# Optimization experiments

Hardware: AMD Instinct MI355X
Metric: run time of the kernel (lower is better)

Reference implementation:

```python
import jax, jax.numpy as jnp
import numpy as np
from jax import lax

NPOINT, RADIUS, NSAMPLE, K_KEY = 64, 1.0, 32, 64

def conv1d(x, W, b):
    # 1x1 Conv1d: x [B,Cin,N], W [Cout,Cin], b [Cout] -> [B,Cout,N]
    return jnp.einsum('bcn,dc->bdn', x, W) + b[None, :, None]

def farthest_point_sample(xyz, npoint):
    # xyz [B,N,3] -> idx [B,npoint]
    B, N, _ = xyz.shape
    dist0 = jnp.full((B, N), 1e10, dtype=xyz.dtype)
    far0 = jnp.zeros((B,), dtype=jnp.int32)
    def body(carry, _):
        dist, far = carry
        centroid = jnp.take_along_axis(xyz, far[:, None, None].astype(jnp.int32), axis=1)  # [B,1,3]
        d = jnp.sum((xyz - centroid) ** 2, -1)
        dist = jnp.minimum(dist, d)
        nxt = jnp.argmax(dist, -1).astype(jnp.int32)
        return (dist, nxt), far
    _, idxs = lax.scan(body, (dist0, far0), None, length=npoint)
    return idxs.T  # [B,npoint]

def ball_query(radius, nsample, xyz, new_xyz):
    # xyz [B,N,3], new_xyz [B,S,3] -> group_idx [B,S,nsample]
    N = xyz.shape[1]
    sqr = jnp.sum((new_xyz[:, :, None, :] - xyz[:, None, :, :]) ** 2, -1)  # [B,S,N]
    gidx = jnp.where(sqr > radius ** 2, N, jnp.arange(N, dtype=jnp.int32)[None, None, :])
    gidx = jnp.sort(gidx, axis=-1)[..., :nsample]
    first = gidx[..., :1]
    gidx = jnp.where(gidx == N, first, gidx)
    return gidx

def sample_and_group(npoint, radius, nsample, xyz, points):
    # xyz [B,N,3], points [B,N,D]
    B = xyz.shape[0]
    fps_idx = farthest_point_sample(xyz, npoint)                     # [B,S]
    bidx = jnp.arange(B)[:, None]
    new_xyz = xyz[bidx, fps_idx]                                     # [B,S,3]
    gidx = ball_query(radius, nsample, xyz, new_xyz)                 # [B,S,ns]
    bidx2 = jnp.arange(B)[:, None, None]
    grouped_xyz = xyz[bidx2, gidx]                                   # [B,S,ns,3]
    grouped_xyz_norm = grouped_xyz - new_xyz[:, :, None, :]
    grouped_points = points[bidx2, gidx]                             # [B,S,ns,D]
    new_points = jnp.concatenate([grouped_xyz_norm, grouped_points], axis=-1)
    return new_xyz, new_points

def setup_inputs() -> dict:
    key = jax.random.key(0)
    ks = jax.random.split(key, 12)
    B, C, N = 8, 6, 65536
    def w(k, co, ci):
        return jax.random.normal(k, (co, ci), jnp.float32) * (1.0 / np.sqrt(ci))
    return {
        'src_pts': jax.random.normal(ks[0], (B, C, N), jnp.float32),
        'tgt_pts': jax.random.normal(ks[1], (B, C, N), jnp.float32),
        'W1': w(ks[2], 32, 6),  'b1': jnp.zeros((32,), jnp.float32),
        'W2': w(ks[3], 64, 32), 'b2': jnp.zeros((64,), jnp.float32),
        'Wa': w(ks[4], 16, 64), 'ba': jnp.zeros((16,), jnp.float32),
        'Wb': w(ks[5], 8, 16),  'bb': jnp.zeros((8,), jnp.float32),
        'Wc': w(ks[6], 1, 8),   'bc': jnp.zeros((1,), jnp.float32),
    }

def reference(src_pts, tgt_pts, W1, b1, W2, b2, Wa, ba, Wb, bb, Wc, bc):
    # feat_extraction_layer: 1x1 conv stack over points -> deep per-point features
    h = jax.nn.relu(conv1d(src_pts, W1, b1))            # [B,32,N]
    deep_feat_pts = jax.nn.relu(conv1d(h, W2, b2))      # [B,64,N]
    # weighting_layer: per-point saliency weight + top-k keypoint indices (1-D, batch-0 idiom)
    w = jax.nn.relu(conv1d(deep_feat_pts, Wa, ba))
    w = jax.nn.relu(conv1d(w, Wb, bb))
    w = jax.nn.softplus(conv1d(w, Wc, bc))              # [B,1,N]
    _, keypts_idx = lax.top_k(w[0, 0], K_KEY)           # [K]
    # irregular keypoint gather (shared index across batch, as in src_pts[:, :, idx])
    src_keypts = src_pts[:, :, keypts_idx].transpose(0, 2, 1)   # [B,K,C]
    # ball-query sample_and_group on keypoints (computed then discarded, as in original)
    _gxyz, _gpts = sample_and_group(NPOINT, RADIUS, NSAMPLE, src_keypts[:, :, :3], src_keypts[:, :, 3:])
    return src_keypts
```

## Files before the change

### kernel.cpp

```cpp
#include <hip/hip_runtime.h>
#include <stdint.h>

#define N_PTS 65536
#define NB1 32768
#define NB2 4096
#define CAND_CAP 4096
#define FCAP 1024
typedef unsigned long long u64;


__global__ __launch_bounds__(256) void zero_kernel(uint4* __restrict__ z, int n4)
{
    const int i = blockIdx.x * 256 + threadIdx.x;
    const uint4 zz = {0u, 0u, 0u, 0u};
    if (i < n4) z[i] = zz;
}

__global__ __launch_bounds__(256, 2) void score_kernel(
    const float* __restrict__ src,
    const float* __restrict__ W1, const float* __restrict__ b1,
    const float* __restrict__ W2, const float* __restrict__ b2,
    const float* __restrict__ Wa, const float* __restrict__ ba,
    const float* __restrict__ Wb, const float* __restrict__ bb,
    const float* __restrict__ Wc, const float* __restrict__ bc,
    float* __restrict__ scores, unsigned* __restrict__ hist1)
{
    __shared__ unsigned histL[NB1 / 2];
    __shared__ __align__(16) float sW1[32 * 8];
    __shared__ __align__(16) float sW2[64 * 32];
    __shared__ __align__(16) float sWaT[64 * 16];
    __shared__ __align__(16) float sWb[8 * 16];
    __shared__ float sb2[64], sba[16], sbb[8], sWc[8], sbc1[1];
    const int t = threadIdx.x;

    {
        uint4* h4 = (uint4*)histL;
        const uint4 zz = {0u, 0u, 0u, 0u};
        #pragma unroll
        for (int i = 0; i < 16; i++) h4[t + 256 * i] = zz;
    }
    {
        const int j = t >> 3, c = t & 7;
        sW1[t] = (c < 6) ? W1[j * 6 + c] : ((c == 6) ? b1[j] : 0.f);
    }
    for (int i = t; i < 2048; i += 256) sW2[i] = W2[i];
    for (int i = t; i < 1024; i += 256) {
        const int j = i >> 4, q = i & 15;
        sWaT[i] = Wa[q * 64 + j];
    }
    if (t < 128) sWb[t] = Wb[t];
    if (t < 64)  sb2[t] = b2[t];
    if (t < 16)  sba[t] = ba[t];
    if (t < 8)   { sbb[t] = bb[t]; sWc[t] = Wc[t]; }
    if (t == 0)  sbc1[0] = bc[0];
    __syncthreads();

    const int p = blockIdx.x * 256 + t;

    float x[6];
    #pragma unroll
    for (int c = 0; c < 6; c++) x[c] = src[c * N_PTS + p];

    float h1[32];
    #pragma unroll
    for (int j = 0; j < 32; j++) {
        const float4 wA = *(const float4*)&sW1[j * 8];
        const float4 wB = *(const float4*)&sW1[j * 8 + 4];
        float a = wB.z;
        a = fmaf(wA.x, x[0], a); a = fmaf(wA.y, x[1], a);
        a = fmaf(wA.z, x[2], a); a = fmaf(wA.w, x[3], a);
        a = fmaf(wB.x, x[4], a); a = fmaf(wB.y, x[5], a);
        h1[j] = fmaxf(a, 0.f);
    }

    float h3[16];
    #pragma unroll
    for (int q = 0; q < 16; q++) h3[q] = sba[q];

    #pragma unroll 1
    for (int jb = 0; jb < 32; jb++) {
        const int j0 = 2 * jb, j1 = j0 + 1;
        const float4* r0 = (const float4*)&sW2[j0 * 32];
        const float4* r1 = (const float4*)&sW2[j1 * 32];
        const float4* wa0 = (const float4*)&sWaT[j0 * 16];
        const float4* wa1 = (const float4*)&sWaT[j1 * 16];
        float4 u[8], v[8], q0[4], q1[4];
        #pragma unroll
        for (int i = 0; i < 8; i++) u[i] = r0[i];
        #pragma unroll
        for (int i = 0; i < 8; i++) v[i] = r1[i];
        #pragma unroll
        for (int i = 0; i < 4; i++) q0[i] = wa0[i];
        #pragma unroll
        for (int i = 0; i < 4; i++) q1[i] = wa1[i];
        const float bj0 = sb2[j0], bj1 = sb2[j1];

        float a0 = 0.f, a1 = 0.f, a2 = 0.f, a3 = 0.f;
        float c0 = 0.f, c1 = 0.f, c2 = 0.f, c3 = 0.f;
        #pragma unroll
        for (int i4 = 0; i4 < 8; i4++) {
            const float h0 = h1[4 * i4 + 0], hh1 = h1[4 * i4 + 1];
            const float h2 = h1[4 * i4 + 2], hh3 = h1[4 * i4 + 3];
            a0 = fmaf(u[i4].x, h0, a0); a1 = fmaf(u[i4].y, hh1, a1);
            a2 = fmaf(u[i4].z, h2, a2); a3 = fmaf(u[i4].w, hh3, a3);
            c0 = fmaf(v[i4].x, h0, c0); c1 = fmaf(v[i4].y, hh1, c1);
            c2 = fmaf(v[i4].z, h2, c2); c3 = fmaf(v[i4].w, hh3, c3);
        }
        const float v0 = fmaxf((a0 + a1) + (a2 + a3) + bj0, 0.f);
        const float v1 = fmaxf((c0 + c1) + (c2 + c3) + bj1, 0.f);
        #pragma unroll
        for (int q4 = 0; q4 < 4; q4++) {
            float t0 = h3[4 * q4 + 0], t1 = h3[4 * q4 + 1];
            float t2 = h3[4 * q4 + 2], t3 = h3[4 * q4 + 3];
            t0 = fmaf(q0[q4].x, v0, t0); t1 = fmaf(q0[q4].y, v0, t1);
            t2 = fmaf(q0[q4].z, v0, t2); t3 = fmaf(q0[q4].w, v0, t3);
            t0 = fmaf(q1[q4].x, v1, t0); t1 = fmaf(q1[q4].y, v1, t1);
            t2 = fmaf(q1[q4].z, v1, t2); t3 = fmaf(q1[q4].w, v1, t3);
            h3[4 * q4 + 0] = t0; h3[4 * q4 + 1] = t1;
            h3[4 * q4 + 2] = t2; h3[4 * q4 + 3] = t3;
        }
    }
    #pragma unroll
    for (int q = 0; q < 16; q++) h3[q] = fmaxf(h3[q], 0.f);

    float z = sbc1[0];
    #pragma unroll
    for (int j = 0; j < 8; j++) {
        const float4* wbr = (const float4*)&sWb[j * 16];
        const float4 w0 = wbr[0], w1 = wbr[1], w2 = wbr[2], w3 = wbr[3];
        const float bj = sbb[j], wc = sWc[j];
        float s0 = bj, s1 = 0.f, s2 = 0.f, s3 = 0.f;
        s0 = fmaf(w0.x, h3[0],  s0); s1 = fmaf(w0.y, h3[1],  s1);
        s2 = fmaf(w0.z, h3[2],  s2); s3 = fmaf(w0.w, h3[3],  s3);
        s0 = fmaf(w1.x, h3[4],  s0); s1 = fmaf(w1.y, h3[5],  s1);
        s2 = fmaf(w1.z, h3[6],  s2); s3 = fmaf(w1.w, h3[7],  s3);
        s0 = fmaf(w2.x, h3[8],  s0); s1 = fmaf(w2.y, h3[9],  s1);
        s2 = fmaf(w2.z, h3[10], s2); s3 = fmaf(w2.w, h3[11], s3);
        s0 = fmaf(w3.x, h3[12], s0); s1 = fmaf(w3.y, h3[13], s1);
        s2 = fmaf(w3.z, h3[14], s2); s3 = fmaf(w3.w, h3[15], s3);
        z = fmaf(wc, fmaxf((s0 + s1) + (s2 + s3), 0.f), z);
    }

    {
        const float sp = fmaxf(z, 0.f) + log1pf(expf(-fabsf(z)));
        scores[p] = sp;
        const unsigned bin = __float_as_uint(sp) >> 16;
        atomicAdd(&histL[bin >> 1], 1u << (16 * (bin & 1)));
    }
    __syncthreads();

    {
        const uint4* h4 = (const uint4*)histL;
        for (int i = t; i < NB1 / 8; i += 256) {
            const uint4 v = h4[i];
            const int b0 = 8 * i;
            const unsigned w[4] = { v.x, v.y, v.z, v.w };
            #pragma unroll
            for (int k = 0; k < 4; k++) {
                const unsigned lo = w[k] & 0xFFFFu;
                const unsigned hi = w[k] >> 16;
                if (lo) atomicAdd(&hist1[b0 + 2 * k + 0], lo);
                if (hi) atomicAdd(&hist1[b0 + 2 * k + 1], hi);
            }
        }
    }
}

__global__ __launch_bounds__(256) void refine_kernel(
    const unsigned* __restrict__ hist1, const float* __restrict__ scores,
    unsigned* __restrict__ hist2, int* __restrict__ meta,
    u64* __restrict__ cand)
{
    __shared__ unsigned csum[256];
    __shared__ unsigned bsum[128];
    __shared__ int sh_c, sh_B;
    __shared__ unsigned sh_tail;
    const int t = threadIdx.x;

    {
        unsigned s = 0;
        const uint4* h4 = (const uint4*)(hist1 + t * 128);
        #pragma unroll
        for (int i = 0; i < 32; i++) {
            const uint4 v = h4[i];
            s += v.x + v.y + v.z + v.w;
        }
        csum[t] = s;
    }
    __syncthreads();
    for (int d = 1; d < 256; d <<= 1) {
        const unsigned v = (t + d < 256) ? csum[t + d] : 0u;
        __syncthreads();
        csum[t] += v;
        __syncthreads();
    }
    {
        const unsigned here = csum[t];
        const unsigned nxt = (t + 1 < 256) ? csum[t + 1] : 0u;
        if (here >= 64u && nxt < 64u) sh_c = t;
    }
    __syncthreads();
    const int cstar = sh_c;
    if (t < 128) bsum[t] = hist1[cstar * 128 + t];
    __syncthreads();
    {
        const unsigned ctail = (cstar + 1 < 256) ? csum[cstar + 1] : 0u;
        for (int d = 1; d < 128; d <<= 1) {
            unsigned v = 0u;
            if (t < 128 && t + d < 128) v = bsum[t + d];
            __syncthreads();
            if (t < 128) bsum[t] += v;
            __syncthreads();
        }
        if (t < 128) {
            const unsigned here = bsum[t] + ctail;
            const unsigned nxt = (t + 1 < 128) ? bsum[t + 1] + ctail : ctail;
            if (here >= 64u && nxt < 64u) { sh_B = cstar * 128 + t; sh_tail = nxt; }
        }
    }
    __syncthreads();
    const unsigned Bstar = (unsigned)sh_B;
    if (blockIdx.x == 0 && t == 0) { meta[0] = sh_B; meta[1] = (int)sh_tail; }

    const float4* s4 = (const float4*)scores;
    const int i = blockIdx.x * 256 + t;
    const float4 v = s4[i];
    const int n0 = 4 * i;
    #pragma unroll
    for (int k = 0; k < 4; k++) {
        const float sv = (k == 0) ? v.x : (k == 1) ? v.y : (k == 2) ? v.z : v.w;
        const unsigned b = __float_as_uint(sv);
        const unsigned hi = b >> 16;
        if (hi >= Bstar) {
            const int p = atomicAdd(&meta[2], 1);
            if (p < CAND_CAP) cand[p] = ((u64)b << 32) | (unsigned)~(n0 + k);
            if (hi == Bstar) atomicAdd(&hist2[(b & 0xFFFFu) >> 4], 1u);
        }
    }
}

__global__ __launch_bounds__(256) void final_kernel(
    const unsigned* __restrict__ hist2, const int* __restrict__ meta,
    const u64* __restrict__ cand, const float* __restrict__ src,
    float* __restrict__ out)
{
    __shared__ unsigned h2[NB2];
    __shared__ unsigned csum[256];
    __shared__ u64 keys[FCAP];
    __shared__ int idxs[64];
    __shared__ int sh_c, sh_T2, sh_cnt;
    const int t = threadIdx.x;
    const unsigned Bstar = (unsigned)meta[0];
    const unsigned tail1 = (unsigned)meta[1];

    {
        uint4* d = (uint4*)h2;
        const uint4* s = (const uint4*)hist2;
        #pragma unroll
        for (int i = 0; i < 4; i++) d[t + 256 * i] = s[t + 256 * i];
    }
    __syncthreads();

    {
        unsigned s = 0;
        #pragma unroll
        for (int i = 0; i < 16; i++) s += h2[t * 16 + i];
        csum[t] = s;
    }
    __syncthreads();
    for (int d = 1; d < 256; d <<= 1) {
        const unsigned v = (t + d < 256) ? csum[t + d] : 0u;
        __syncthreads();
        csum[t] += v;
        __syncthreads();
    }
    {
        const unsigned here = tail1 + csum[t];
        const unsigned nxt = tail1 + ((t + 1 < 256) ? csum[t + 1] : 0u);
        if (here >= 64u && nxt < 64u) sh_c = t;
    }
    __syncthreads();
    {
        const int c2 = sh_c;
        if (t == 0) {
            unsigned acc = tail1 + ((c2 + 1 < 256) ? csum[c2 + 1] : 0u);
            int T2 = c2 * 16;
            for (int b = c2 * 16 + 15; b >= c2 * 16; b--) {
                acc += h2[b];
                if (acc >= 64u) { T2 = b; break; }
            }
            sh_T2 = T2;
            sh_cnt = 0;
        }
    }
    __syncthreads();
    const unsigned T2 = (unsigned)sh_T2;

    int count = meta[2];
    if (count > CAND_CAP) count = CAND_CAP;
    for (int i = t; i < count; i += 256) {
        const u64 key = cand[i];
        const unsigned b = (unsigned)(key >> 32);
        const unsigned hi = b >> 16;
        if (hi > Bstar || ((b & 0xFFFFu) >> 4) >= T2) {
            const int p = atomicAdd(&sh_cnt, 1);
            if (p < FCAP) keys[p] = key;
        }
    }
    __syncthreads();

    int fcnt = sh_cnt;
    if (fcnt > FCAP) fcnt = FCAP;
    for (int i = t; i < fcnt; i += 256) {
        const u64 me = keys[i];
        int r = 0;
        for (int j = 0; j < fcnt; j++) r += (keys[j] > me);
        if (r < 64) idxs[r] = (int)~(unsigned)(me & 0xFFFFFFFFu);
    }
    __syncthreads();

    for (int e = t; e < 3072; e += 256) {
        const int b  = e / 384;
        const int rr = e % 384;
        const int kk = rr / 6;
        const int c  = rr % 6;
        out[e] = src[(b * 6 + c) * N_PTS + idxs[kk]];
    }
}

extern "C" void kernel_launch(void* const* d_in, const int* in_sizes, int n_in,
                              void* d_out, int out_size, void* d_ws, size_t ws_size,
                              hipStream_t stream)
{
    const float* src = (const float*)d_in[0];
    const float* W1 = (const float*)d_in[2];
    const float* b1 = (const float*)d_in[3];
    const float* W2 = (const float*)d_in[4];
    const float* b2 = (const float*)d_in[5];
    const float* Wa = (const float*)d_in[6];
    const float* ba = (const float*)d_in[7];
    const float* Wb = (const float*)d_in[8];
    const float* bb = (const float*)d_in[9];
    const float* Wc = (const float*)d_in[10];
    const float* bc = (const float*)d_in[11];

    char* ws = (char*)d_ws;
    float*    scores = (float*)ws;
    unsigned* hist1  = (unsigned*)(ws + 256 * 1024);
    unsigned* hist2  = (unsigned*)(ws + 384 * 1024);
    int*      meta   = (int*)(ws + 400 * 1024);
    u64*      cand   = (u64*)(ws + 408 * 1024);
    float*    out    = (float*)d_out;

    const int n4 = (NB1 + NB2 + 16) / 4;
    zero_kernel<<<(n4 + 255) / 256, 256, 0, stream>>>((uint4*)hist1, n4);
    score_kernel<<<256, 256, 0, stream>>>(src, W1, b1, W2, b2, Wa, ba,
                                          Wb, bb, Wc, bc, scores, hist1);
    refine_kernel<<<64, 256, 0, stream>>>(hist1, scores, hist2, meta, cand);
    final_kernel<<<1, 256, 0, stream>>>(hist2, meta, cand, src, out);
}
```

Baseline: 157.1 us.

## Pre-pack MLP weights in zero kernel and read them directly from global memory

The zero kernel gets an extra block that packs W1/b1, W2, transposed Wa and b2 into one interleaved buffer in the workspace. The score kernel drops its per-block LDS staging of weights and reads the uniform packed weights straight from global memory, where they should become scalar or cached loads. This removes LDS fill work and LDS weight reads per block, but depends on global loads of uniform data being served quickly from cache.

```diff
diff --git a/kernel.cpp b/kernel.cpp
--- a/kernel.cpp
+++ b/kernel.cpp
@@ -6,31 +6,52 @@
 #define NB2 4096
 #define CAND_CAP 4096
 #define FCAP 1024
+#define PK_FLOATS (256 + 32 * 112)
 typedef unsigned long long u64;
 
 
-__global__ __launch_bounds__(256) void zero_kernel(uint4* __restrict__ z, int n4)
-{
-    const int i = blockIdx.x * 256 + threadIdx.x;
+__global__ __launch_bounds__(256) void zero_pack_kernel(
+    uint4* __restrict__ z, int n4,
+    const float* __restrict__ W1, const float* __restrict__ b1,
+    const float* __restrict__ W2, const float* __restrict__ b2,
+    const float* __restrict__ Wa, float* __restrict__ pk)
+{
+    const int t = threadIdx.x;
+    const int i = blockIdx.x * 256 + t;
     const uint4 zz = {0u, 0u, 0u, 0u};
     if (i < n4) z[i] = zz;
+
+    if (blockIdx.x == gridDim.x - 1) {
+        for (int e = t; e < PK_FLOATS; e += 256) {
+            float v;
+            if (e < 256) {
+                const int j = e >> 3, c = e & 7;
+                v = (c < 6) ? W1[j * 6 + c] : ((c == 6) ? b1[j] : 0.f);
+            } else {
+                const int r = e - 256;
+                const int jb = r / 112, k = r % 112;
+                if (k < 32)       v = W2[(2 * jb) * 32 + k];
+                else if (k < 64)  v = W2[(2 * jb + 1) * 32 + (k - 32)];
+                else if (k < 80)  v = Wa[(k - 64) * 64 + 2 * jb];
+                else if (k < 96)  v = Wa[(k - 80) * 64 + (2 * jb + 1)];
+                else if (k == 96) v = b2[2 * jb];
+                else if (k == 97) v = b2[2 * jb + 1];
+                else              v = 0.f;
+            }
+            pk[e] = v;
+        }
+    }
 }
 
 __global__ __launch_bounds__(256, 2) void score_kernel(
     const float* __restrict__ src,
-    const float* __restrict__ W1, const float* __restrict__ b1,
-    const float* __restrict__ W2, const float* __restrict__ b2,
-    const float* __restrict__ Wa, const float* __restrict__ ba,
+    const float* __restrict__ pk,
+    const float* __restrict__ ba,
     const float* __restrict__ Wb, const float* __restrict__ bb,
     const float* __restrict__ Wc, const float* __restrict__ bc,
     float* __restrict__ scores, unsigned* __restrict__ hist1)
 {
     __shared__ unsigned histL[NB1 / 2];
-    __shared__ __align__(16) float sW1[32 * 8];
-    __shared__ __align__(16) float sW2[64 * 32];
-    __shared__ __align__(16) float sWaT[64 * 16];
-    __shared__ __align__(16) float sWb[8 * 16];
-    __shared__ float sb2[64], sba[16], sbb[8], sWc[8], sbc1[1];
     const int t = threadIdx.x;
 
     {
@@ -39,20 +60,6 @@
         #pragma unroll
         for (int i = 0; i < 16; i++) h4[t + 256 * i] = zz;
     }
-    {
-        const int j = t >> 3, c = t & 7;
-        sW1[t] = (c < 6) ? W1[j * 6 + c] : ((c == 6) ? b1[j] : 0.f);
-    }
-    for (int i = t; i < 2048; i += 256) sW2[i] = W2[i];
-    for (int i = t; i < 1024; i += 256) {
-        const int j = i >> 4, q = i & 15;
-        sWaT[i] = Wa[q * 64 + j];
-    }
-    if (t < 128) sWb[t] = Wb[t];
-    if (t < 64)  sb2[t] = b2[t];
-    if (t < 16)  sba[t] = ba[t];
-    if (t < 8)   { sbb[t] = bb[t]; sWc[t] = Wc[t]; }
-    if (t == 0)  sbc1[0] = bc[0];
     __syncthreads();
 
     const int p = blockIdx.x * 256 + t;
@@ -61,11 +68,12 @@
     #pragma unroll
     for (int c = 0; c < 6; c++) x[c] = src[c * N_PTS + p];
 
+    const float4* w1p = (const float4*)pk;
     float h1[32];
     #pragma unroll
     for (int j = 0; j < 32; j++) {
-        const float4 wA = *(const float4*)&sW1[j * 8];
-        const float4 wB = *(const float4*)&sW1[j * 8 + 4];
+        const float4 wA = w1p[2 * j];
+        const float4 wB = w1p[2 * j + 1];
         float a = wB.z;
         a = fmaf(wA.x, x[0], a); a = fmaf(wA.y, x[1], a);
         a = fmaf(wA.z, x[2], a); a = fmaf(wA.w, x[3], a);
@@ -73,27 +81,29 @@
         h1[j] = fmaxf(a, 0.f);
     }
 
+    const float4* bap = (const float4*)ba;
     float h3[16];
     #pragma unroll
-    for (int q = 0; q < 16; q++) h3[q] = sba[q];
+    for (int q4 = 0; q4 < 4; q4++) {
+        const float4 b4 = bap[q4];
+        h3[4 * q4 + 0] = b4.x; h3[4 * q4 + 1] = b4.y;
+        h3[4 * q4 + 2] = b4.z; h3[4 * q4 + 3] = b4.w;
+    }
 
     #pragma unroll 1
     for (int jb = 0; jb < 32; jb++) {
-        const int j0 = 2 * jb, j1 = j0 + 1;
-        const float4* r0 = (const float4*)&sW2[j0 * 32];
-        const float4* r1 = (const float4*)&sW2[j1 * 32];
-        const float4* wa0 = (const float4*)&sWaT[j0 * 16];
-        const float4* wa1 = (const float4*)&sWaT[j1 * 16];
+        const float4* blk = (const float4*)(pk + 256 + jb * 112);
         float4 u[8], v[8], q0[4], q1[4];
         #pragma unroll
-        for (int i = 0; i < 8; i++) u[i] = r0[i];
-        #pragma unroll
-        for (int i = 0; i < 8; i++) v[i] = r1[i];
-        #pragma unroll
-        for (int i = 0; i < 4; i++) q0[i] = wa0[i];
-        #pragma unroll
-        for (int i = 0; i < 4; i++) q1[i] = wa1[i];
-        const float bj0 = sb2[j0], bj1 = sb2[j1];
+        for (int i = 0; i < 8; i++) u[i] = blk[i];
+        #pragma unroll
+        for (int i = 0; i < 8; i++) v[i] = blk[8 + i];
+        #pragma unroll
+        for (int i = 0; i < 4; i++) q0[i] = blk[16 + i];
+        #pragma unroll
+        for (int i = 0; i < 4; i++) q1[i] = blk[20 + i];
+        const float bj0 = pk[256 + jb * 112 + 96];
+        const float bj1 = pk[256 + jb * 112 + 97];
 
         float a0 = 0.f, a1 = 0.f, a2 = 0.f, a3 = 0.f;
         float c0 = 0.f, c1 = 0.f, c2 = 0.f, c3 = 0.f;
@@ -123,12 +133,12 @@
     #pragma unroll
     for (int q = 0; q < 16; q++) h3[q] = fmaxf(h3[q], 0.f);
 
-    float z = sbc1[0];
+    float z = bc[0];
     #pragma unroll
     for (int j = 0; j < 8; j++) {
-        const float4* wbr = (const float4*)&sWb[j * 16];
+        const float4* wbr = (const float4*)(Wb + j * 16);
         const float4 w0 = wbr[0], w1 = wbr[1], w2 = wbr[2], w3 = wbr[3];
-        const float bj = sbb[j], wc = sWc[j];
+        const float bj = bb[j], wc = Wc[j];
         float s0 = bj, s1 = 0.f, s2 = 0.f, s3 = 0.f;
         s0 = fmaf(w0.x, h3[0],  s0); s1 = fmaf(w0.y, h3[1],  s1);
         s2 = fmaf(w0.z, h3[2],  s2); s3 = fmaf(w0.w, h3[3],  s3);
@@ -350,12 +360,14 @@
     unsigned* hist2  = (unsigned*)(ws + 384 * 1024);
     int*      meta   = (int*)(ws + 400 * 1024);
     u64*      cand   = (u64*)(ws + 408 * 1024);
+    float*    pk     = (float*)(ws + 440 * 1024);
     float*    out    = (float*)d_out;
 
     const int n4 = (NB1 + NB2 + 16) / 4;
-    zero_kernel<<<(n4 + 255) / 256, 256, 0, stream>>>((uint4*)hist1, n4);
-    score_kernel<<<256, 256, 0, stream>>>(src, W1, b1, W2, b2, Wa, ba,
-                                          Wb, bb, Wc, bc, scores, hist1);
+    zero_pack_kernel<<<(n4 + 255) / 256 + 1, 256, 0, stream>>>(
+        (uint4*)hist1, n4, W1, b1, W2, b2, Wa, pk);
+    score_kernel<<<256, 256, 0, stream>>>(src, pk, ba, Wb, bb, Wc, bc,
+                                          scores, hist1);
     refine_kernel<<<64, 256, 0, stream>>>(hist1, scores, hist2, meta, cand);
     final_kernel<<<1, 256, 0, stream>>>(hist2, meta, cand, src, out);
 }
```

New measurement: 165.5 us. 5.3% more time.

## Split each point's MLP across 4 lanes and move histogram to separate kernel

Applied to the files above, without the earlier changes.

The score kernel now assigns four threads per point. Each lane computes a quarter of the 64-channel hidden layer, and partial 16-channel sums are reduced with xor shuffles. Weights are repacked into a per-pair block layout, and the grid grows to 1024 blocks with higher occupancy bounds. The score histogram moves out into a new kernel with a full 32-bit local histogram. This trades a larger grid and an extra launch with a scores round-trip for more parallelism on only 256 blocks of work.

```diff
diff --git a/kernel.cpp b/kernel.cpp
--- a/kernel.cpp
+++ b/kernel.cpp
@@ -16,46 +16,48 @@
     if (i < n4) z[i] = zz;
 }
 
-__global__ __launch_bounds__(256, 2) void score_kernel(
+__global__ __launch_bounds__(256, 4) void score_kernel(
     const float* __restrict__ src,
     const float* __restrict__ W1, const float* __restrict__ b1,
     const float* __restrict__ W2, const float* __restrict__ b2,
     const float* __restrict__ Wa, const float* __restrict__ ba,
     const float* __restrict__ Wb, const float* __restrict__ bb,
     const float* __restrict__ Wc, const float* __restrict__ bc,
-    float* __restrict__ scores, unsigned* __restrict__ hist1)
-{
-    __shared__ unsigned histL[NB1 / 2];
+    float* __restrict__ scores)
+{
     __shared__ __align__(16) float sW1[32 * 8];
-    __shared__ __align__(16) float sW2[64 * 32];
-    __shared__ __align__(16) float sWaT[64 * 16];
+    __shared__ __align__(16) float sJB[32 * 116];
     __shared__ __align__(16) float sWb[8 * 16];
-    __shared__ float sb2[64], sba[16], sbb[8], sWc[8], sbc1[1];
+    __shared__ __align__(16) float sba[16];
+    __shared__ __align__(16) float sbb[8];
+    __shared__ __align__(16) float sWc[8];
+    __shared__ float sbc1[1];
     const int t = threadIdx.x;
 
-    {
-        uint4* h4 = (uint4*)histL;
-        const uint4 zz = {0u, 0u, 0u, 0u};
-        #pragma unroll
-        for (int i = 0; i < 16; i++) h4[t + 256 * i] = zz;
-    }
     {
         const int j = t >> 3, c = t & 7;
         sW1[t] = (c < 6) ? W1[j * 6 + c] : ((c == 6) ? b1[j] : 0.f);
     }
-    for (int i = t; i < 2048; i += 256) sW2[i] = W2[i];
-    for (int i = t; i < 1024; i += 256) {
-        const int j = i >> 4, q = i & 15;
-        sWaT[i] = Wa[q * 64 + j];
+    for (int i = t; i < 32 * 116; i += 256) {
+        const int jb = i / 116, k = i % 116;
+        float v = 0.f;
+        if (k < 32)       v = W2[(2 * jb) * 32 + k];
+        else if (k < 64)  v = W2[(2 * jb + 1) * 32 + (k - 32)];
+        else if (k < 80)  v = Wa[(k - 64) * 64 + 2 * jb];
+        else if (k < 96)  v = Wa[(k - 80) * 64 + (2 * jb + 1)];
+        else if (k == 96) v = b2[2 * jb];
+        else if (k == 97) v = b2[2 * jb + 1];
+        sJB[i] = v;
     }
     if (t < 128) sWb[t] = Wb[t];
-    if (t < 64)  sb2[t] = b2[t];
     if (t < 16)  sba[t] = ba[t];
     if (t < 8)   { sbb[t] = bb[t]; sWc[t] = Wc[t]; }
     if (t == 0)  sbc1[0] = bc[0];
     __syncthreads();
 
-    const int p = blockIdx.x * 256 + t;
+    const int gid = blockIdx.x * 256 + t;
+    const int p   = gid >> 2;
+    const int sub = t & 3;
 
     float x[6];
     #pragma unroll
@@ -75,25 +77,23 @@
 
     float h3[16];
     #pragma unroll
-    for (int q = 0; q < 16; q++) h3[q] = sba[q];
+    for (int q = 0; q < 16; q++) h3[q] = (sub == 0) ? sba[q] : 0.f;
 
     #pragma unroll 1
-    for (int jb = 0; jb < 32; jb++) {
-        const int j0 = 2 * jb, j1 = j0 + 1;
-        const float4* r0 = (const float4*)&sW2[j0 * 32];
-        const float4* r1 = (const float4*)&sW2[j1 * 32];
-        const float4* wa0 = (const float4*)&sWaT[j0 * 16];
-        const float4* wa1 = (const float4*)&sWaT[j1 * 16];
+    for (int i = 0; i < 8; i++) {
+        const int jb = 4 * i + sub;
+        const float* blk = &sJB[jb * 116];
+        const float4* b4 = (const float4*)blk;
         float4 u[8], v[8], q0[4], q1[4];
         #pragma unroll
-        for (int i = 0; i < 8; i++) u[i] = r0[i];
-        #pragma unroll
-        for (int i = 0; i < 8; i++) v[i] = r1[i];
-        #pragma unroll
-        for (int i = 0; i < 4; i++) q0[i] = wa0[i];
-        #pragma unroll
-        for (int i = 0; i < 4; i++) q1[i] = wa1[i];
-        const float bj0 = sb2[j0], bj1 = sb2[j1];
+        for (int k = 0; k < 8; k++) u[k] = b4[k];
+        #pragma unroll
+        for (int k = 0; k < 8; k++) v[k] = b4[8 + k];
+        #pragma unroll
+        for (int k = 0; k < 4; k++) q0[k] = b4[16 + k];
+        #pragma unroll
+        for (int k = 0; k < 4; k++) q1[k] = b4[20 + k];
+        const float bj0 = blk[96], bj1 = blk[97];
 
         float a0 = 0.f, a1 = 0.f, a2 = 0.f, a3 = 0.f;
         float c0 = 0.f, c1 = 0.f, c2 = 0.f, c3 = 0.f;
@@ -120,8 +120,14 @@
             h3[4 * q4 + 2] = t2; h3[4 * q4 + 3] = t3;
         }
     }
-    #pragma unroll
-    for (int q = 0; q < 16; q++) h3[q] = fmaxf(h3[q], 0.f);
+
+    #pragma unroll
+    for (int q = 0; q < 16; q++) {
+        float o = h3[q];
+        o += __shfl_xor(o, 1);
+        o += __shfl_xor(o, 2);
+        h3[q] = fmaxf(o, 0.f);
+    }
 
     float z = sbc1[0];
     #pragma unroll
@@ -141,28 +147,41 @@
         z = fmaf(wc, fmaxf((s0 + s1) + (s2 + s3), 0.f), z);
     }
 
-    {
+    if (sub == 0) {
         const float sp = fmaxf(z, 0.f) + log1pf(expf(-fabsf(z)));
         scores[p] = sp;
-        const unsigned bin = __float_as_uint(sp) >> 16;
-        atomicAdd(&histL[bin >> 1], 1u << (16 * (bin & 1)));
-    }
-    __syncthreads();
-
-    {
-        const uint4* h4 = (const uint4*)histL;
-        for (int i = t; i < NB1 / 8; i += 256) {
-            const uint4 v = h4[i];
-            const int b0 = 8 * i;
-            const unsigned w[4] = { v.x, v.y, v.z, v.w };
-            #pragma unroll
-            for (int k = 0; k < 4; k++) {
-                const unsigned lo = w[k] & 0xFFFFu;
-                const unsigned hi = w[k] >> 16;
-                if (lo) atomicAdd(&hist1[b0 + 2 * k + 0], lo);
-                if (hi) atomicAdd(&hist1[b0 + 2 * k + 1], hi);
-            }
-        }
+    }
+}
+
+__global__ __launch_bounds__(256, 1) void hist_kernel(
+    const float* __restrict__ scores, unsigned* __restrict__ hist1)
+{
+    __shared__ unsigned histL[NB1];
+    const int t = threadIdx.x;
+    {
+        uint4* h4 = (uint4*)histL;
+        const uint4 zz = {0u, 0u, 0u, 0u};
+        #pragma unroll
+        for (int i = 0; i < 32; i++) h4[t + 256 * i] = zz;
+    }
+    __syncthreads();
+
+    const float4 v = ((const float4*)scores)[blockIdx.x * 256 + t];
+    atomicAdd(&histL[__float_as_uint(v.x) >> 16], 1u);
+    atomicAdd(&histL[__float_as_uint(v.y) >> 16], 1u);
+    atomicAdd(&histL[__float_as_uint(v.z) >> 16], 1u);
+    atomicAdd(&histL[__float_as_uint(v.w) >> 16], 1u);
+    __syncthreads();
+
+    const uint4* h4 = (const uint4*)histL;
+    #pragma unroll 1
+    for (int k = 0; k < 32; k++) {
+        const uint4 vv = h4[t + 256 * k];
+        const int b0 = 4 * (t + 256 * k);
+        if (vv.x) atomicAdd(&hist1[b0 + 0], vv.x);
+        if (vv.y) atomicAdd(&hist1[b0 + 1], vv.y);
+        if (vv.z) atomicAdd(&hist1[b0 + 2], vv.z);
+        if (vv.w) atomicAdd(&hist1[b0 + 3], vv.w);
     }
 }
 
@@ -354,8 +373,9 @@
 
     const int n4 = (NB1 + NB2 + 16) / 4;
     zero_kernel<<<(n4 + 255) / 256, 256, 0, stream>>>((uint4*)hist1, n4);
-    score_kernel<<<256, 256, 0, stream>>>(src, W1, b1, W2, b2, Wa, ba,
-                                          Wb, bb, Wc, bc, scores, hist1);
+    score_kernel<<<1024, 256, 0, stream>>>(src, W1, b1, W2, b2, Wa, ba,
+                                           Wb, bb, Wc, bc, scores);
+    hist_kernel<<<64, 256, 0, stream>>>(scores, hist1);
     refine_kernel<<<64, 256, 0, stream>>>(hist1, scores, hist2, meta, cand);
     final_kernel<<<1, 256, 0, stream>>>(hist2, meta, cand, src, out);
 }
```

New measurement: 141.3 us. 10.1% less time.
